# Kernel tuning notes

Hardware: AMD Instinct MI355X
Metric: run time of the kernel (lower is better)

The kernel has to match this reference:

```python
import jax, jax.numpy as jnp
import numpy as np

N_NODES = 100000
N_EDGES = 1600000
D_IN = 128
D_OUT = 128


def setup_inputs() -> dict:
    key = jax.random.key(0)
    k1, k2, k3, k4, k5 = jax.random.split(key, 5)
    h = jax.random.normal(k1, (N_NODES, D_IN), dtype=jnp.float32)
    src = jax.random.randint(k2, (N_EDGES,), 0, N_NODES, dtype=jnp.int64)
    dst = jax.random.randint(k3, (N_EDGES,), 0, N_NODES, dtype=jnp.int64)
    W = jax.random.normal(k4, (2 * D_IN, D_OUT), dtype=jnp.float32) * (1.0 / np.sqrt(2 * D_IN))
    b = jax.random.normal(k5, (D_OUT,), dtype=jnp.float32) * 0.01
    return {"h": h, "src": src, "dst": dst, "W": W, "b": b}


def reference(h, src, dst, W, b):
    # copy_u + mean: scatter-mean of source features onto destination nodes
    msg_sum = jax.ops.segment_sum(h[src], dst, num_segments=N_NODES)  # [N, D_IN]
    deg = jax.ops.segment_sum(jnp.ones((src.shape[0],), h.dtype), dst, num_segments=N_NODES)  # [N]
    h_N = jnp.where(deg[:, None] > 0, msg_sum / jnp.maximum(deg, 1.0)[:, None], 0.0)
    h_total = jnp.concatenate([h, h_N], axis=1)  # [N, 2*D_IN]
    return h_total @ W + b
```

## Files before the change

kernel.cpp:

```cpp
#include <hip/hip_runtime.h>
#include <stdint.h>

#define N_NODES 100000
#define D 128
#define BN 64
#define NB ((N_NODES + BN - 1) / BN)
#define EPB 4096
#define CAP 1536
#define HPAD 136

typedef short bf16x8 __attribute__((ext_vector_type(8)));
typedef float f32x4 __attribute__((ext_vector_type(4)));

__device__ __forceinline__ unsigned short f2bf(float f) {
    unsigned int x = __float_as_uint(f);
    unsigned int r = x + 0x7fffu + ((x >> 16) & 1u);
    return (unsigned short)(r >> 16);
}
__device__ __forceinline__ float blo(unsigned int u) { return __uint_as_float(u << 16); }
__device__ __forceinline__ float bhi(unsigned int u) { return __uint_as_float(u & 0xffff0000u); }

__global__ __launch_bounds__(256) void prep_k(
    const float* __restrict__ h, unsigned short* __restrict__ h_bf,
    const float* __restrict__ W, unsigned short* __restrict__ Wf,
    const int* __restrict__ src, const int* __restrict__ dst,
    int* __restrict__ cnt, unsigned int* __restrict__ pairs,
    int n_edges, int partb)
{
    __shared__ int hist[NB];
    __shared__ int lc[NB];

    int bid = blockIdx.x;
    int t = threadIdx.x;

    if (bid < partb) {
        for (int i = t; i < NB; i += 256) { hist[i] = 0; lc[i] = 0; }
        __syncthreads();
        int base = bid * EPB;
        int lim = n_edges - base; if (lim > EPB) lim = EPB; if (lim < 0) lim = 0;
        for (int i = t; i < lim; i += 256)
            atomicAdd(&hist[dst[base + i] >> 6], 1);
        __syncthreads();
        for (int i = t; i < NB; i += 256) {
            int c = hist[i];
            hist[i] = c ? atomicAdd(&cnt[i], c) : 0;
        }
        __syncthreads();
        for (int i = t; i < lim; i += 256) {
            int e = base + i;
            int d = dst[e], b = d >> 6;
            int slot = atomicAdd(&lc[b], 1);
            int off = hist[b] + slot;
            if (off < CAP)
                pairs[(size_t)b * CAP + off] =
                    (unsigned int)src[e] | ((unsigned int)(d & 63) << 17);
        }
    } else if (bid < partb + 16) {
        int gid = (bid - partb) * 256 + t;
        if (gid < 64 * 64) {
            int f = gid >> 6, l = gid & 63;
            int kt = f >> 3, ct = f & 7;
            int n = ct * 16 + (l & 15);
            int kb = kt * 32 + (l >> 4) * 8;
            #pragma unroll
            for (int j = 0; j < 8; ++j)
                Wf[(size_t)f * 512 + l * 8 + j] = f2bf(W[(size_t)(kb + j) * D + n]);
        }
    } else {
        size_t base = ((size_t)(bid - partb - 16) * 256 + t) * 4;
        if (base < (size_t)N_NODES * D) {
            float4 v = *(const float4*)(h + base);
            ushort4 o;
            o.x = f2bf(v.x); o.y = f2bf(v.y); o.z = f2bf(v.z); o.w = f2bf(v.w);
            *(ushort4*)(h_bf + base) = o;
        }
    }
}

__global__ __launch_bounds__(512, 8) void aggemm_k(
    const unsigned short* __restrict__ h_bf, const unsigned int* __restrict__ pairs,
    const int* __restrict__ cnt_g, const unsigned short* __restrict__ Wf,
    const float* __restrict__ bias, float* __restrict__ out)
{
    __shared__ unsigned int lp[CAP];
    __shared__ unsigned int srt[CAP];
    __shared__ int counts[BN];
    __shared__ int startp[BN];
    __shared__ int cursor[BN];
    __shared__ unsigned short hNs[BN][HPAD];

    int t = threadIdx.x;
    int b = blockIdx.x;
    int wv = t >> 6, l = t & 63;
    size_t e0 = (size_t)b * CAP;
    int cnt = cnt_g[b];
    if (cnt > CAP) cnt = CAP;

    if (t < BN) counts[t] = 0;
    __syncthreads();

    for (int i = t; i < cnt; i += 512) {
        unsigned int p = pairs[e0 + i];
        lp[i] = p;
        atomicAdd(&counts[p >> 17], 1);
    }
    __syncthreads();

    if (t < BN) startp[t] = counts[t];
    __syncthreads();
    #pragma unroll
    for (int off = 1; off < BN; off <<= 1) {
        int v = 0;
        if (t < BN && t >= off) v = startp[t - off];
        __syncthreads();
        if (t < BN) startp[t] += v;
        __syncthreads();
    }
    if (t < BN) {
        int ex = startp[t] - counts[t];
        startp[t] = ex;
        cursor[t] = ex;
    }
    __syncthreads();

    for (int i = t; i < cnt; i += 512) {
        unsigned int p = lp[i];
        int s = atomicAdd(&cursor[p >> 17], 1);
        srt[s] = p & 0x1FFFFu;
    }
    __syncthreads();

    int q = l >> 4, lq = l & 15;
    int nbase = b * BN;
    #pragma unroll
    for (int p2 = 0; p2 < 2; ++p2) {
        int nl = p2 * 32 + wv * 4 + q;
        int dg = counts[nl], s0 = startp[nl];
        float a0 = 0.f, a1 = 0.f, a2 = 0.f, a3 = 0.f;
        float a4 = 0.f, a5 = 0.f, a6 = 0.f, a7 = 0.f;
        int i = 0;
        for (; i + 4 <= dg; i += 4) {
            int s0i = srt[s0 + i],     s1i = srt[s0 + i + 1];
            int s2i = srt[s0 + i + 2], s3i = srt[s0 + i + 3];
            uint4 u0 = *(const uint4*)(h_bf + (size_t)s0i * D + lq * 8);
            uint4 u1 = *(const uint4*)(h_bf + (size_t)s1i * D + lq * 8);
            uint4 u2 = *(const uint4*)(h_bf + (size_t)s2i * D + lq * 8);
            uint4 u3 = *(const uint4*)(h_bf + (size_t)s3i * D + lq * 8);
            a0 += (blo(u0.x) + blo(u1.x)) + (blo(u2.x) + blo(u3.x));
            a1 += (bhi(u0.x) + bhi(u1.x)) + (bhi(u2.x) + bhi(u3.x));
            a2 += (blo(u0.y) + blo(u1.y)) + (blo(u2.y) + blo(u3.y));
            a3 += (bhi(u0.y) + bhi(u1.y)) + (bhi(u2.y) + bhi(u3.y));
            a4 += (blo(u0.z) + blo(u1.z)) + (blo(u2.z) + blo(u3.z));
            a5 += (bhi(u0.z) + bhi(u1.z)) + (bhi(u2.z) + bhi(u3.z));
            a6 += (blo(u0.w) + blo(u1.w)) + (blo(u2.w) + blo(u3.w));
            a7 += (bhi(u0.w) + bhi(u1.w)) + (bhi(u2.w) + bhi(u3.w));
        }
        for (; i < dg; ++i) {
            uint4 u = *(const uint4*)(h_bf + (size_t)srt[s0 + i] * D + lq * 8);
            a0 += blo(u.x); a1 += bhi(u.x);
            a2 += blo(u.y); a3 += bhi(u.y);
            a4 += blo(u.z); a5 += bhi(u.z);
            a6 += blo(u.w); a7 += bhi(u.w);
        }
        float invd = dg > 0 ? 1.0f / (float)dg : 0.f;
        uint4 o;
        o.x = ((unsigned int)f2bf(a1 * invd) << 16) | f2bf(a0 * invd);
        o.y = ((unsigned int)f2bf(a3 * invd) << 16) | f2bf(a2 * invd);
        o.z = ((unsigned int)f2bf(a5 * invd) << 16) | f2bf(a4 * invd);
        o.w = ((unsigned int)f2bf(a7 * invd) << 16) | f2bf(a6 * invd);
        *(uint4*)(&hNs[nl][lq * 8]) = o;
    }
    __syncthreads();

    int rt = wv >> 1, ch = wv & 1;
    int lrow = l & 15, lqd = l >> 4;
    int lr = rt * 16 + lrow;
    int r0 = nbase + lr; if (r0 > N_NODES - 1) r0 = N_NODES - 1;

    f32x4 acc[4];
    #pragma unroll
    for (int c = 0; c < 4; ++c) acc[c] = (f32x4){0.f, 0.f, 0.f, 0.f};

    const unsigned short* wf_lane = Wf + l * 8;

    #pragma unroll
    for (int kt = 0; kt < 8; ++kt) {
        int ko = (kt & 3) * 32 + lqd * 8;
        bf16x8 a;
        if (kt < 4)
            a = *(const bf16x8*)(h_bf + (size_t)r0 * D + ko);
        else
            a = *(const bf16x8*)(&hNs[lr][ko]);
        #pragma unroll
        for (int c = 0; c < 4; ++c) {
            int ct = ch * 4 + c;
            bf16x8 bfr = *(const bf16x8*)(wf_lane + (size_t)(kt * 8 + ct) * 512);
            acc[c] = __builtin_amdgcn_mfma_f32_16x16x32_bf16(a, bfr, acc[c], 0, 0, 0);
        }
    }

    int col = l & 15, qd = l >> 4;
    #pragma unroll
    for (int c = 0; c < 4; ++c) {
        int ct = ch * 4 + c;
        float bv = bias[ct * 16 + col];
        #pragma unroll
        for (int r = 0; r < 4; ++r) {
            int row = nbase + rt * 16 + qd * 4 + r;
            if (row < N_NODES)
                out[(size_t)row * D + ct * 16 + col] = acc[c][r] + bv;
        }
    }
}


extern "C" void kernel_launch(void* const* d_in, const int* in_sizes, int n_in,
                              void* d_out, int out_size, void* d_ws, size_t ws_size,
                              hipStream_t stream) {
    const float* h  = (const float*)d_in[0];
    const int* src  = (const int*)d_in[1];
    const int* dst  = (const int*)d_in[2];
    const float* W  = (const float*)d_in[3];
    const float* b  = (const float*)d_in[4];
    float* out      = (float*)d_out;
    int n_edges = in_sizes[1];

    char* ws = (char*)d_ws;
    unsigned short* h_bf  = (unsigned short*)ws;
    unsigned int* pairs   = (unsigned int*)(h_bf + (size_t)N_NODES * D);
    unsigned short* Wf    = (unsigned short*)(pairs + (size_t)NB * CAP);
    int* cnt              = (int*)(Wf + 64 * 512);

    hipMemsetAsync(cnt, 0, NB * sizeof(int), stream);

    int partb = (n_edges + EPB - 1) / EPB;
    int cblocks = (int)(((size_t)N_NODES * D / 4 + 255) / 256);
    hipLaunchKernelGGL(prep_k, dim3(partb + 16 + cblocks), dim3(256), 0, stream,
                       h, h_bf, W, Wf, src, dst, cnt, pairs, n_edges, partb);

    hipLaunchKernelGGL(aggemm_k, dim3(NB), dim3(512), 0, stream,
                       h_bf, pairs, cnt, Wf, b, out);
}
```

Before: 227.8 us.

## Replicate per-bucket edge counters and sort edges by destination and source range

The global per-bucket atomic counter is split into four replicas, picked by partition block index, so fewer blocks contend on the same counter, and each replica writes to its own sub-array of pairs. The aggregation kernel reads the four segments back and sorts with a 512-bin key (destination node plus the high bits of the source index) instead of 64 bins. Within each destination the gathers therefore run in ascending source order, which should improve cache locality. The cost is a wider prefix scan with more barriers, and each replica is capped at 448 edges, which could drop edges if the destinations are skewed.

```diff
diff --git a/kernel.cpp b/kernel.cpp
--- a/kernel.cpp
+++ b/kernel.cpp
@@ -6,8 +6,11 @@
 #define BN 64
 #define NB ((N_NODES + BN - 1) / BN)
 #define EPB 4096
+#define NR 4
+#define CAPR 448
 #define CAP 1536
 #define HPAD 136
+#define NK 512
 
 typedef short bf16x8 __attribute__((ext_vector_type(8)));
 typedef float f32x4 __attribute__((ext_vector_type(4)));
@@ -41,9 +44,10 @@
         for (int i = t; i < lim; i += 256)
             atomicAdd(&hist[dst[base + i] >> 6], 1);
         __syncthreads();
+        int rep = bid & (NR - 1);
         for (int i = t; i < NB; i += 256) {
             int c = hist[i];
-            hist[i] = c ? atomicAdd(&cnt[i], c) : 0;
+            hist[i] = c ? atomicAdd(&cnt[i * NR + rep], c) : 0;
         }
         __syncthreads();
         for (int i = t; i < lim; i += 256) {
@@ -51,8 +55,8 @@
             int d = dst[e], b = d >> 6;
             int slot = atomicAdd(&lc[b], 1);
             int off = hist[b] + slot;
-            if (off < CAP)
-                pairs[(size_t)b * CAP + off] =
+            if (off < CAPR)
+                pairs[((size_t)b * NR + rep) * CAPR + off] =
                     (unsigned int)src[e] | ((unsigned int)(d & 63) << 17);
         }
     } else if (bid < partb + 16) {
@@ -84,48 +88,64 @@
 {
     __shared__ unsigned int lp[CAP];
     __shared__ unsigned int srt[CAP];
+    __shared__ int cnt2[NK];
+    __shared__ int ps[NK];
+    __shared__ int cur2[NK];
     __shared__ int counts[BN];
     __shared__ int startp[BN];
-    __shared__ int cursor[BN];
     __shared__ unsigned short hNs[BN][HPAD];
 
     int t = threadIdx.x;
     int b = blockIdx.x;
     int wv = t >> 6, l = t & 63;
-    size_t e0 = (size_t)b * CAP;
-    int cnt = cnt_g[b];
-    if (cnt > CAP) cnt = CAP;
-
-    if (t < BN) counts[t] = 0;
-    __syncthreads();
-
-    for (int i = t; i < cnt; i += 512) {
-        unsigned int p = pairs[e0 + i];
-        lp[i] = p;
-        atomicAdd(&counts[p >> 17], 1);
-    }
-    __syncthreads();
-
-    if (t < BN) startp[t] = counts[t];
-    __syncthreads();
-    #pragma unroll
-    for (int off = 1; off < BN; off <<= 1) {
-        int v = 0;
-        if (t < BN && t >= off) v = startp[t - off];
-        __syncthreads();
-        if (t < BN) startp[t] += v;
-        __syncthreads();
-    }
-    if (t < BN) {
-        int ex = startp[t] - counts[t];
-        startp[t] = ex;
-        cursor[t] = ex;
-    }
+
+    int segc[NR], sego[NR];
+    {
+        int tot = 0;
+        #pragma unroll
+        for (int r = 0; r < NR; ++r) {
+            int c = cnt_g[b * NR + r];
+            if (c > CAPR) c = CAPR;
+            if (tot + c > CAP) c = CAP - tot;
+            sego[r] = tot; segc[r] = c; tot += c;
+        }
+    }
+
+    cnt2[t] = 0;
+    __syncthreads();
+
+    #pragma unroll
+    for (int r = 0; r < NR; ++r) {
+        const unsigned int* psg = pairs + ((size_t)b * NR + r) * CAPR;
+        int c = segc[r], o = sego[r];
+        for (int i = t; i < c; i += 512) {
+            unsigned int p = psg[i];
+            lp[o + i] = p;
+            atomicAdd(&cnt2[p >> 14], 1);
+        }
+    }
+    int cnt = sego[NR - 1] + segc[NR - 1];
+    __syncthreads();
+
+    ps[t] = cnt2[t];
+    __syncthreads();
+    #pragma unroll
+    for (int off = 1; off < NK; off <<= 1) {
+        int v = (t >= off) ? ps[t - off] : 0;
+        __syncthreads();
+        ps[t] += v;
+        __syncthreads();
+    }
+    int excl = ps[t] - cnt2[t];
+    cur2[t] = excl;
+    if ((t & 7) == 0) startp[t >> 3] = excl;
+    __syncthreads();
+    if ((t & 7) == 7) counts[t >> 3] = ps[t] - startp[t >> 3];
     __syncthreads();
 
     for (int i = t; i < cnt; i += 512) {
         unsigned int p = lp[i];
-        int s = atomicAdd(&cursor[p >> 17], 1);
+        int s = atomicAdd(&cur2[p >> 14], 1);
         srt[s] = p & 0x1FFFFu;
     }
     __syncthreads();
@@ -228,10 +248,10 @@
     char* ws = (char*)d_ws;
     unsigned short* h_bf  = (unsigned short*)ws;
     unsigned int* pairs   = (unsigned int*)(h_bf + (size_t)N_NODES * D);
-    unsigned short* Wf    = (unsigned short*)(pairs + (size_t)NB * CAP);
+    unsigned short* Wf    = (unsigned short*)(pairs + (size_t)NB * NR * CAPR);
     int* cnt              = (int*)(Wf + 64 * 512);
 
-    hipMemsetAsync(cnt, 0, NB * sizeof(int), stream);
+    hipMemsetAsync(cnt, 0, NB * NR * sizeof(int), stream);
 
     int partb = (n_edges + EPB - 1) / EPB;
     int cblocks = (int)(((size_t)N_NODES * D / 4 + 255) / 256);
```

Result: faster. 222.1 us (-2.5%).
